# Kernel optimization log

Hardware: AMD Instinct MI355X
Metric: run time of the kernel (lower is better)

## Reference

```python
import jax, jax.numpy as jnp
import numpy as np

B, CIN, COUT, ATOM = 128, 32, 128, 64
ITER_NUM = 5


def setup_inputs() -> dict:
    key = jax.random.key(0)
    x = jax.random.normal(key, (B, CIN, COUT, ATOM), dtype=jnp.float32)
    gamma = jnp.ones((1, CIN, 1, 1), dtype=jnp.float32)
    beta = jnp.zeros((1, CIN, 1, 1), dtype=jnp.float32)
    return {"x": x, "gamma": gamma, "beta": beta}


def _iter_norm_inv_sqrt(sigma, iter_num):
    # Newton-Schulz iterative inverse square root (IterNorm).
    trace = jnp.trace(sigma)
    sigma_n = sigma / trace  # trace-normalized so ||I - sigma_n|| < 1
    p = jnp.eye(sigma.shape[0], dtype=sigma.dtype)
    for _ in range(iter_num):
        p = 0.5 * (3.0 * p - p @ p @ p @ sigma_n)
    return p * jax.lax.rsqrt(trace)


def reference(x, gamma, beta):
    # x: [B, caps_in, caps_out, atom]; center per caps_in over (batch, caps_out, atom)
    mean = jnp.mean(x, axis=(0, 2, 3), keepdims=True)
    centered = x - mean
    norm_dim = COUT * ATOM * B
    # [B, caps_out, atom, caps_in] -> [N, caps_in]
    c = jnp.transpose(centered, (0, 2, 3, 1)).reshape(-1, CIN)
    sigma = (c.T @ c) / (jnp.float32(norm_dim) - 1.0)  # [caps_in, caps_in]
    inv_sqrt = _iter_norm_inv_sqrt(sigma, ITER_NUM)
    d = c @ inv_sqrt
    d = d.reshape(-1, COUT, ATOM, CIN)
    d = jnp.transpose(d, (0, 3, 1, 2))  # back to [B, caps_in, caps_out, atom]
    return d * gamma + beta
```

## Files before the change

kernel.cpp:

```cpp
#include <hip/hip_runtime.h>

constexpr int CIN  = 32;
constexpr int COUT = 128;
constexpr int ATOM = 64;
constexpr int BB   = 128;
constexpr int COLS_PER_B = COUT * ATOM;
constexpr long long NTOT = (long long)BB * COLS_PER_B;
constexpr float NTOTF = 1048576.0f;

typedef float f32x4 __attribute__((ext_vector_type(4)));

constexpr int TK    = 256;
constexpr int PAD   = 260;
constexpr int GRID1 = 1024;
constexpr int TILES = 4096;
constexpr int TPB   = TILES / GRID1;


__global__ __launch_bounds__(256) void stats_kernel(const float* __restrict__ x,
                                                    float* __restrict__ acc) {
    __shared__ float tile[CIN * PAD];
    __shared__ float ssum[CIN];
    const int t = threadIdx.x;
    const int w = t >> 6;
    const int l = t & 63;
    const int ti = l >> 3;
    const int tj = l & 7;

    float accg[4][4] = {};
    float asum[4] = {0.f, 0.f, 0.f, 0.f};
    if (t < CIN) ssum[t] = 0.f;

    for (int tt = 0; tt < TPB; ++tt) {
        const int tileid = blockIdx.x * TPB + tt;
        const int b = tileid >> 5;
        const int col0 = (tileid & 31) << 8;
        const float* xb = x + (size_t)b * CIN * COLS_PER_B + col0;

        __syncthreads();
        #pragma unroll
        for (int rr = 0; rr < 8; ++rr) {
            const int row = rr * 4 + w;
            float4 v = *(const float4*)(xb + (size_t)row * COLS_PER_B + l * 4);
            *(float4*)(&tile[row * PAD + l * 4]) = v;
        }
        __syncthreads();

        #pragma unroll
        for (int s = 0; s < 16; ++s) {
            const int k = w * 64 + s * 4;
            float4 av[4], bv[4];
            #pragma unroll
            for (int d = 0; d < 4; ++d) av[d] = *(const float4*)(&tile[(ti + 8 * d) * PAD + k]);
            #pragma unroll
            for (int d = 0; d < 4; ++d) bv[d] = *(const float4*)(&tile[(tj + 8 * d) * PAD + k]);
            #pragma unroll
            for (int di = 0; di < 4; ++di) {
                asum[di] += av[di].x + av[di].y + av[di].z + av[di].w;
                #pragma unroll
                for (int dj = 0; dj < 4; ++dj) {
                    accg[di][dj] += av[di].x * bv[dj].x + av[di].y * bv[dj].y
                                  + av[di].z * bv[dj].z + av[di].w * bv[dj].w;
                }
            }
        }
    }

    __syncthreads();
    #pragma unroll
    for (int di = 0; di < 4; ++di)
        #pragma unroll
        for (int dj = 0; dj < 4; ++dj)
            tile[w * 1024 + (ti + 8 * di) * 32 + (tj + 8 * dj)] = accg[di][dj];
    if (tj == 0) {
        #pragma unroll
        for (int di = 0; di < 4; ++di) atomicAdd(&ssum[ti + 8 * di], asum[di]);
    }
    __syncthreads();
    #pragma unroll
    for (int q = 0; q < 4; ++q) {
        const int idx = t + q * 256;
        const float v = tile[idx] + tile[1024 + idx] + tile[2048 + idx] + tile[3072 + idx];
        atomicAdd(&acc[idx], v);
    }
    if (t < CIN) atomicAdd(&acc[1024 + t], ssum[t]);
}

__global__ __launch_bounds__(1024) void newton_kernel(const float* __restrict__ acc,
                                                      const float* __restrict__ gamma,
                                                      const float* __restrict__ beta,
                                                      float* __restrict__ outp) {
    __shared__ float sn[32 * 33], p[32 * 33], t1[32 * 33], t2[32 * 33];
    __shared__ float mean[32], diag[32], trs[1];
    const int t = threadIdx.x;
    const int i = t >> 5, j = t & 31;

    if (t < 32) mean[t] = acc[1024 + t] * (1.0f / NTOTF);
    __syncthreads();
    const float sig = (acc[t] - NTOTF * mean[i] * mean[j]) * (1.0f / (NTOTF - 1.0f));
    if (i == j) diag[i] = sig;
    __syncthreads();
    if (t == 0) {
        float tr = 0.f;
        for (int k = 0; k < 32; ++k) tr += diag[k];
        trs[0] = tr;
    }
    __syncthreads();
    const float tr = trs[0];
    sn[i * 33 + j] = sig / tr;
    p[i * 33 + j]  = (i == j) ? 1.0f : 0.0f;
    __syncthreads();

    for (int it = 0; it < 5; ++it) {
        float a = 0.f;
        #pragma unroll
        for (int k = 0; k < 32; ++k) a += p[i * 33 + k] * p[k * 33 + j];
        t1[i * 33 + j] = a;
        __syncthreads();
        float c = 0.f;
        #pragma unroll
        for (int k = 0; k < 32; ++k) c += t1[i * 33 + k] * p[k * 33 + j];
        t2[i * 33 + j] = c;
        __syncthreads();
        float v = 0.f;
        #pragma unroll
        for (int k = 0; k < 32; ++k) v += t2[i * 33 + k] * sn[k * 33 + j];
        const float pn = 1.5f * p[i * 33 + j] - 0.5f * v;
        __syncthreads();
        p[i * 33 + j] = pn;
        __syncthreads();
    }

    const float r = rsqrtf(tr);
    const float wv = p[i * 33 + j] * r * gamma[j];
    t1[i * 33 + j] = wv;
    outp[t] = wv;
    __syncthreads();
    if (t < 32) {
        float bb = beta[t];
        for (int k = 0; k < 32; ++k) bb -= mean[k] * t1[k * 33 + t];
        outp[1024 + t] = bb;
    }
}

__global__ __launch_bounds__(256) void apply_kernel(const float* __restrict__ x,
                                                    const float* __restrict__ wm,
                                                    float* __restrict__ out) {
    const size_t tid  = (size_t)blockIdx.x * 256 + threadIdx.x;
    const size_t col4 = tid * 4;
    const size_t b    = col4 >> 13;
    const size_t c    = col4 & 8191;
    const float* xp = x + b * (size_t)(CIN * COLS_PER_B) + c;
    float* op       = out + b * (size_t)(CIN * COLS_PER_B) + c;

    float4 vals[32];
    #pragma unroll
    for (int i = 0; i < 32; ++i) vals[i] = *(const float4*)(xp + (size_t)i * COLS_PER_B);

    #pragma unroll
    for (int jb = 0; jb < 4; ++jb) {
        float4 accv[8];
        #pragma unroll
        for (int jj = 0; jj < 8; ++jj) {
            const float bv = wm[1024 + jb * 8 + jj];
            accv[jj] = make_float4(bv, bv, bv, bv);
        }
        #pragma unroll
        for (int i = 0; i < 32; ++i) {
            #pragma unroll
            for (int jj = 0; jj < 8; ++jj) {
                const float sv = wm[i * 32 + jb * 8 + jj];
                accv[jj].x += vals[i].x * sv;
                accv[jj].y += vals[i].y * sv;
                accv[jj].z += vals[i].z * sv;
                accv[jj].w += vals[i].w * sv;
            }
        }
        #pragma unroll
        for (int jj = 0; jj < 8; ++jj) {
            f32x4 v = { accv[jj].x, accv[jj].y, accv[jj].z, accv[jj].w };
            __builtin_nontemporal_store(v, (f32x4*)(op + (size_t)(jb * 8 + jj) * COLS_PER_B));
        }
    }
}

extern "C" void kernel_launch(void* const* d_in, const int* in_sizes, int n_in,
                              void* d_out, int out_size, void* d_ws, size_t ws_size,
                              hipStream_t stream) {
    const float* x     = (const float*)d_in[0];
    const float* gamma = (const float*)d_in[1];
    const float* beta  = (const float*)d_in[2];
    float* out = (float*)d_out;
    float* acc = (float*)d_ws;

    (void)hipMemsetAsync(acc, 0, 1056 * sizeof(float), stream);
    stats_kernel<<<GRID1, 256, 0, stream>>>(x, acc);
    newton_kernel<<<1, 1024, 0, stream>>>(acc, gamma, beta, acc + 1056);
    apply_kernel<<<(NTOT / 4) / 256, 256, 0, stream>>>(x, acc + 1056, out);
}
```

Before: 435.4 us.

## Double-buffer stats tile loads via registers; shrink apply per-thread width to float2

The stats kernel now prefetches the next tile into registers while computing on the current shared-memory tile, and halves the grid so each block processes more tiles. This is meant to hide global load latency behind the Gram-matrix FMAs. The apply kernel switches from float4 to float2 per thread with launch_bounds(256,4), cutting register pressure from the 32-element staging array so occupancy rises. The cost is more threads and narrower memory transactions in apply, and fewer blocks in stats.

```diff
diff --git a/kernel.cpp b/kernel.cpp
--- a/kernel.cpp
+++ b/kernel.cpp
@@ -8,11 +8,11 @@
 constexpr long long NTOT = (long long)BB * COLS_PER_B;
 constexpr float NTOTF = 1048576.0f;
 
-typedef float f32x4 __attribute__((ext_vector_type(4)));
+typedef float f32x2 __attribute__((ext_vector_type(2)));
 
 constexpr int TK    = 256;
 constexpr int PAD   = 260;
-constexpr int GRID1 = 1024;
+constexpr int GRID1 = 512;
 constexpr int TILES = 4096;
 constexpr int TPB   = TILES / GRID1;
 
@@ -31,21 +31,25 @@
     float asum[4] = {0.f, 0.f, 0.f, 0.f};
     if (t < CIN) ssum[t] = 0.f;
 
-    for (int tt = 0; tt < TPB; ++tt) {
-        const int tileid = blockIdx.x * TPB + tt;
+    const int tile0 = blockIdx.x * TPB;
+    auto srcp = [&](int tileid, int row) -> const float* {
         const int b = tileid >> 5;
         const int col0 = (tileid & 31) << 8;
-        const float* xb = x + (size_t)b * CIN * COLS_PER_B + col0;
-
-        __syncthreads();
-        #pragma unroll
-        for (int rr = 0; rr < 8; ++rr) {
-            const int row = rr * 4 + w;
-            float4 v = *(const float4*)(xb + (size_t)row * COLS_PER_B + l * 4);
-            *(float4*)(&tile[row * PAD + l * 4]) = v;
-        }
-        __syncthreads();
-
+        return x + (size_t)b * CIN * COLS_PER_B + (size_t)row * COLS_PER_B + col0 + l * 4;
+    };
+
+    float4 stg[8];
+    #pragma unroll
+    for (int rr = 0; rr < 8; ++rr) stg[rr] = *(const float4*)srcp(tile0, rr * 4 + w);
+    #pragma unroll
+    for (int rr = 0; rr < 8; ++rr) *(float4*)(&tile[(rr * 4 + w) * PAD + l * 4]) = stg[rr];
+    __syncthreads();
+
+    for (int tt = 0; tt < TPB; ++tt) {
+        if (tt + 1 < TPB) {
+            #pragma unroll
+            for (int rr = 0; rr < 8; ++rr) stg[rr] = *(const float4*)srcp(tile0 + tt + 1, rr * 4 + w);
+        }
         #pragma unroll
         for (int s = 0; s < 16; ++s) {
             const int k = w * 64 + s * 4;
@@ -64,9 +68,14 @@
                 }
             }
         }
-    }
-
-    __syncthreads();
+        __syncthreads();
+        if (tt + 1 < TPB) {
+            #pragma unroll
+            for (int rr = 0; rr < 8; ++rr) *(float4*)(&tile[(rr * 4 + w) * PAD + l * 4]) = stg[rr];
+        }
+        __syncthreads();
+    }
+
     #pragma unroll
     for (int di = 0; di < 4; ++di)
         #pragma unroll
@@ -143,27 +152,27 @@
     }
 }
 
-__global__ __launch_bounds__(256) void apply_kernel(const float* __restrict__ x,
-                                                    const float* __restrict__ wm,
-                                                    float* __restrict__ out) {
+__global__ __launch_bounds__(256, 4) void apply_kernel(const float* __restrict__ x,
+                                                       const float* __restrict__ wm,
+                                                       float* __restrict__ out) {
     const size_t tid  = (size_t)blockIdx.x * 256 + threadIdx.x;
-    const size_t col4 = tid * 4;
-    const size_t b    = col4 >> 13;
-    const size_t c    = col4 & 8191;
+    const size_t col2 = tid * 2;
+    const size_t b    = col2 >> 13;
+    const size_t c    = col2 & 8191;
     const float* xp = x + b * (size_t)(CIN * COLS_PER_B) + c;
     float* op       = out + b * (size_t)(CIN * COLS_PER_B) + c;
 
-    float4 vals[32];
-    #pragma unroll
-    for (int i = 0; i < 32; ++i) vals[i] = *(const float4*)(xp + (size_t)i * COLS_PER_B);
+    float2 vals[32];
+    #pragma unroll
+    for (int i = 0; i < 32; ++i) vals[i] = *(const float2*)(xp + (size_t)i * COLS_PER_B);
 
     #pragma unroll
     for (int jb = 0; jb < 4; ++jb) {
-        float4 accv[8];
+        float2 accv[8];
         #pragma unroll
         for (int jj = 0; jj < 8; ++jj) {
             const float bv = wm[1024 + jb * 8 + jj];
-            accv[jj] = make_float4(bv, bv, bv, bv);
+            accv[jj] = make_float2(bv, bv);
         }
         #pragma unroll
         for (int i = 0; i < 32; ++i) {
@@ -172,14 +181,12 @@
                 const float sv = wm[i * 32 + jb * 8 + jj];
                 accv[jj].x += vals[i].x * sv;
                 accv[jj].y += vals[i].y * sv;
-                accv[jj].z += vals[i].z * sv;
-                accv[jj].w += vals[i].w * sv;
             }
         }
         #pragma unroll
         for (int jj = 0; jj < 8; ++jj) {
-            f32x4 v = { accv[jj].x, accv[jj].y, accv[jj].z, accv[jj].w };
-            __builtin_nontemporal_store(v, (f32x4*)(op + (size_t)(jb * 8 + jj) * COLS_PER_B));
+            f32x2 v = { accv[jj].x, accv[jj].y };
+            __builtin_nontemporal_store(v, (f32x2*)(op + (size_t)(jb * 8 + jj) * COLS_PER_B));
         }
     }
 }
@@ -196,5 +203,5 @@
     (void)hipMemsetAsync(acc, 0, 1056 * sizeof(float), stream);
     stats_kernel<<<GRID1, 256, 0, stream>>>(x, acc);
     newton_kernel<<<1, 1024, 0, stream>>>(acc, gamma, beta, acc + 1056);
-    apply_kernel<<<(NTOT / 4) / 256, 256, 0, stream>>>(x, acc + 1056, out);
-}
+    apply_kernel<<<(NTOT / 2) / 256, 256, 0, stream>>>(x, acc + 1056, out);
+}
```

Result: slower. 507.5 us (+16.6%).
